# Kernel optimization log

Measured on AMD Instinct MI355X. Metric: run time of the kernel, lower is better.

The kernel has to match this reference:

```python
import jax, jax.numpy as jnp
import numpy as np

N_NODES = 50000
N_EDGES = 800000


def spmm(edge_src, edge_dst, edge_weight, h):
    # out[i] = sum over edges (src->dst=i) of w * h[src]  == adj @ h
    msgs = h[edge_src] * edge_weight[:, None]  # [E, D]
    return jax.ops.segment_sum(msgs, edge_dst, num_segments=N_NODES)


def setup_inputs() -> dict:
    key = jax.random.key(0)
    ks = jax.random.split(key, 12)
    x = jax.random.normal(ks[0], (N_NODES, 512), dtype=jnp.float32)
    edge_src = jax.random.randint(ks[1], (N_EDGES,), 0, N_NODES, dtype=jnp.int32)
    edge_dst = jax.random.randint(ks[2], (N_EDGES,), 0, N_NODES, dtype=jnp.int32)
    edge_weight = jax.random.uniform(ks[3], (N_EDGES,), dtype=jnp.float32)
    def init_w(k, fin, fout):
        s = 1.0 / np.sqrt(fout)
        return jax.random.uniform(k, (fin, fout), minval=-s, maxval=s, dtype=jnp.float32)
    W1 = init_w(ks[4], 512, 512); b1 = jnp.zeros((512,), jnp.float32)
    W2 = init_w(ks[5], 512, 256); b2 = jnp.zeros((256,), jnp.float32)
    W3 = init_w(ks[6], 256, 128); b3 = jnp.zeros((128,), jnp.float32)
    W4 = init_w(ks[7], 128, 64);  b4 = jnp.zeros((64,), jnp.float32)
    return {"x": x, "edge_src": edge_src, "edge_dst": edge_dst,
            "edge_weight": edge_weight, "W1": W1, "b1": b1, "W2": W2,
            "b2": b2, "W3": W3, "b3": b3, "W4": W4, "b4": b4}


def reference(x, edge_src, edge_dst, edge_weight, W1, b1, W2, b2, W3, b3, W4, b4):
    # GraphConvolution: out = adj @ (x @ W) + b ; dropout is identity in eval mode
    def gc(h, W, b):
        return spmm(edge_src, edge_dst, edge_weight, h @ W) + b
    h = jax.nn.relu(gc(x, W1, b1))
    h = jax.nn.relu(gc(h, W2, b2))
    h = jax.nn.relu(gc(h, W3, b3))
    emb = gc(h, W4, b4)
    return emb
```

## Files before the change

### kernel.cpp

```cpp
#include <hip/hip_runtime.h>

#define NN 50000
#define NE 800000
#define SCAN_BLOCKS 196

typedef __attribute__((ext_vector_type(8))) short short8;
typedef __attribute__((ext_vector_type(4))) float float4v;

struct us4 { unsigned short x, y, z, w; };
struct us8 { unsigned short v[8]; };

__device__ __forceinline__ unsigned short f2bf(float f) {
    unsigned u = __float_as_uint(f);
    unsigned r = (u + 0x7FFF + ((u >> 16) & 1)) >> 16;
    return (unsigned short)r;
}

__device__ __forceinline__ float bf2f(unsigned short u) {
    return __uint_as_float((unsigned)u << 16);
}

__device__ __forceinline__ void gload_lds16(const unsigned short* g, unsigned short* l) {
    __builtin_amdgcn_global_load_lds(
        (const __attribute__((address_space(1))) unsigned int*)g,
        (__attribute__((address_space(3))) unsigned int*)l,
        16, 0, 0);
}

template <int BM, int BN, int WM, int WN, int OUTBF>
__global__ __launch_bounds__(256) void gemm_mfma(const unsigned short* __restrict__ A,
                                                 const unsigned short* __restrict__ Bt,
                                                 void* __restrict__ Cv,
                                                 int N, int K, int M) {
    constexpr int BK = 32;
    constexpr int MT = WM / 16;
    constexpr int NT = WN / 16;
    constexpr int WCOLS = BN / WN;

    __shared__ __align__(16) unsigned short As[BM * BK];
    __shared__ __align__(16) unsigned short Bs[BN * BK];

    const int tid = threadIdx.x;
    const int lane = tid & 63;
    const int wid = tid >> 6;
    const int col16 = lane & 15;
    const int q = lane >> 4;
    const int wr = (wid / WCOLS) * WM;
    const int wc = (wid % WCOLS) * WN;
    const int rowBase = blockIdx.y * BM;
    const int colBase = blockIdx.x * BN;

    const int srow = lane >> 2;
    const int scol = (lane & 3) * 8;

    float4v acc[MT][NT];
#pragma unroll
    for (int t = 0; t < MT; ++t)
#pragma unroll
        for (int u = 0; u < NT; ++u)
            acc[t][u] = (float4v)0.f;

    for (int k0 = 0; k0 < K; k0 += BK) {
        __syncthreads();
#pragma unroll
        for (int l = wid; l < BM / 16; l += 4) {
            int row = rowBase + 16 * l + srow;
            row = row < N ? row : N - 1;
            gload_lds16(A + (size_t)row * K + k0 + scol, &As[l * 512]);
        }
#pragma unroll
        for (int l = wid; l < BN / 16; l += 4) {
            const int row = colBase + 16 * l + srow;
            gload_lds16(Bt + (size_t)row * K + k0 + scol, &Bs[l * 512]);
        }
        __syncthreads();

        short8 a[MT], b[NT];
#pragma unroll
        for (int t = 0; t < MT; ++t)
            a[t] = *(const short8*)&As[(wr + t * 16 + col16) * BK + q * 8];
#pragma unroll
        for (int u = 0; u < NT; ++u)
            b[u] = *(const short8*)&Bs[(wc + u * 16 + col16) * BK + q * 8];
#pragma unroll
        for (int t = 0; t < MT; ++t)
#pragma unroll
            for (int u = 0; u < NT; ++u)
                acc[t][u] = __builtin_amdgcn_mfma_f32_16x16x32_bf16(a[t], b[u], acc[t][u], 0, 0, 0);
    }

#pragma unroll
    for (int t = 0; t < MT; ++t) {
        const int row0 = rowBase + wr + t * 16 + q * 4;
#pragma unroll
        for (int u = 0; u < NT; ++u) {
            const int col = colBase + wc + u * 16 + col16;
#pragma unroll
            for (int r = 0; r < 4; ++r) {
                const int row = row0 + r;
                if (row < N) {
                    if (OUTBF)
                        ((unsigned short*)Cv)[(size_t)row * M + col] = f2bf(acc[t][u][r]);
                    else
                        ((float*)Cv)[(size_t)row * M + col] = acc[t][u][r];
                }
            }
        }
    }
}

__global__ void cvt_f32_bf16(const float* __restrict__ in, unsigned short* __restrict__ out,
                             long long n4) {
    long long i = (long long)blockIdx.x * blockDim.x + threadIdx.x;
    const long long stride = (long long)gridDim.x * blockDim.x;
    for (; i < n4; i += stride) {
        const float4 v = *(const float4*)&in[i * 4];
        us4 o = {f2bf(v.x), f2bf(v.y), f2bf(v.z), f2bf(v.w)};
        *(us4*)&out[i * 4] = o;
    }
}

__global__ void cvt_transpose(const float* __restrict__ W, unsigned short* __restrict__ Wt,
                              int K, int M) {
    int idx = blockIdx.x * blockDim.x + threadIdx.x;
    const int total = K * M;
    if (idx < total) {
        const int k = idx / M;
        const int m = idx % M;
        Wt[(size_t)m * K + k] = f2bf(W[idx]);
    }
}

__global__ void zero_counts(int* __restrict__ counts) {
    int i = blockIdx.x * blockDim.x + threadIdx.x;
    if (i < NN) counts[i] = 0;
}

__global__ void hist_dst(const int* __restrict__ dst, int* __restrict__ counts) {
    int i = blockIdx.x * blockDim.x + threadIdx.x;
    const int stride = gridDim.x * blockDim.x;
    for (; i < NE; i += stride) atomicAdd(&counts[dst[i]], 1);
}

__global__ __launch_bounds__(256) void scan_partial(const int* __restrict__ counts,
                                                    int* __restrict__ partials) {
    __shared__ int r[256];
    const int t = threadIdx.x;
    const int i = blockIdx.x * 256 + t;
    r[t] = (i < NN) ? counts[i] : 0;
    __syncthreads();
    for (int s = 128; s > 0; s >>= 1) {
        if (t < s) r[t] += r[t + s];
        __syncthreads();
    }
    if (t == 0) partials[blockIdx.x] = r[0];
}

__global__ __launch_bounds__(256) void scan_base(const int* __restrict__ partials,
                                                 int* __restrict__ bases,
                                                 int* __restrict__ offs) {
    __shared__ int s[256];
    const int t = threadIdx.x;
    const int v = (t < SCAN_BLOCKS) ? partials[t] : 0;
    s[t] = v;
    __syncthreads();
    for (int off = 1; off < 256; off <<= 1) {
        int x = (t >= off) ? s[t - off] : 0;
        __syncthreads();
        s[t] += x;
        __syncthreads();
    }
    if (t < SCAN_BLOCKS) bases[t] = s[t] - v;
    if (t == 255) offs[NN] = s[255];
}

__global__ __launch_bounds__(256) void scan_final(int* __restrict__ counts,
                                                  const int* __restrict__ bases,
                                                  int* __restrict__ offs) {
    __shared__ int s[256];
    const int t = threadIdx.x;
    const int i = blockIdx.x * 256 + t;
    const int v = (i < NN) ? counts[i] : 0;
    s[t] = v;
    __syncthreads();
    for (int off = 1; off < 256; off <<= 1) {
        int x = (t >= off) ? s[t - off] : 0;
        __syncthreads();
        s[t] += x;
        __syncthreads();
    }
    if (i < NN) {
        const int e = bases[blockIdx.x] + s[t] - v;
        offs[i] = e;
        counts[i] = e;
    }
}

__global__ void fill_csr(const int* __restrict__ src, const int* __restrict__ dst,
                         const float* __restrict__ w, int* __restrict__ cursor,
                         int* __restrict__ csr_src, float* __restrict__ csr_w) {
    int i = blockIdx.x * blockDim.x + threadIdx.x;
    const int stride = gridDim.x * blockDim.x;
    for (; i < NE; i += stride) {
        const int p = atomicAdd(&cursor[dst[i]], 1);
        csr_src[p] = src[i];
        csr_w[p] = w[i];
    }
}

template <int D, int RELU, int OUTBF>
__global__ __launch_bounds__(256) void spmm_gather(const int* __restrict__ offs,
                                                   const int* __restrict__ csr_src,
                                                   const float* __restrict__ csr_w,
                                                   const unsigned short* __restrict__ hp,
                                                   const float* __restrict__ bias,
                                                   void* __restrict__ outv) {
    constexpr int TPN = D / 8;
    constexpr int NPB = 256 / TPN;
    const int tid = threadIdx.x;
    const int node = blockIdx.x * NPB + tid / TPN;
    const int d = (tid % TPN) * 8;
    if (node >= NN) return;
    const int beg = offs[node];
    const int end = offs[node + 1];

    float acc[8] = {};
    int j = beg;
    for (; j + 2 <= end; j += 2) {
        const int s0 = csr_src[j];
        const int s1 = csr_src[j + 1];
        const float w0 = csr_w[j];
        const float w1 = csr_w[j + 1];
        const us8 h0 = *(const us8*)&hp[(long long)s0 * D + d];
        const us8 h1 = *(const us8*)&hp[(long long)s1 * D + d];
#pragma unroll
        for (int k = 0; k < 8; ++k)
            acc[k] += w0 * bf2f(h0.v[k]) + w1 * bf2f(h1.v[k]);
    }
    if (j < end) {
        const int s0 = csr_src[j];
        const float w0 = csr_w[j];
        const us8 h0 = *(const us8*)&hp[(long long)s0 * D + d];
#pragma unroll
        for (int k = 0; k < 8; ++k)
            acc[k] += w0 * bf2f(h0.v[k]);
    }
#pragma unroll
    for (int k = 0; k < 8; ++k) {
        acc[k] += bias[d + k];
        if (RELU) acc[k] = fmaxf(acc[k], 0.f);
    }
    if (OUTBF) {
        us8 o;
#pragma unroll
        for (int k = 0; k < 8; ++k) o.v[k] = f2bf(acc[k]);
        *(us8*)((unsigned short*)outv + (long long)node * D + d) = o;
    } else {
        float* op = (float*)outv + (long long)node * D + d;
        *(float4*)op = make_float4(acc[0], acc[1], acc[2], acc[3]);
        *(float4*)(op + 4) = make_float4(acc[4], acc[5], acc[6], acc[7]);
    }
}

extern "C" void kernel_launch(void* const* d_in, const int* in_sizes, int n_in,
                              void* d_out, int out_size, void* d_ws, size_t ws_size,
                              hipStream_t stream) {
    const float* x    = (const float*)d_in[0];
    const int*   esrc = (const int*)d_in[1];
    const int*   edst = (const int*)d_in[2];
    const float* ew   = (const float*)d_in[3];
    const float* W1 = (const float*)d_in[4];  const float* b1 = (const float*)d_in[5];
    const float* W2 = (const float*)d_in[6];  const float* b2 = (const float*)d_in[7];
    const float* W3 = (const float*)d_in[8];  const float* b3 = (const float*)d_in[9];
    const float* W4 = (const float*)d_in[10]; const float* b4 = (const float*)d_in[11];
    float* out = (float*)d_out;

    char* ws = (char*)d_ws;
    int*   offs    = (int*)ws;                    ws += (NN + 1) * sizeof(int);
    int*   counts  = (int*)ws;                    ws += NN * sizeof(int);
    int*   partials= (int*)ws;                    ws += 256 * sizeof(int);
    int*   bases   = (int*)ws;                    ws += 256 * sizeof(int);
    int*   csr_src = (int*)ws;                    ws += NE * sizeof(int);
    float* csr_w   = (float*)ws;                  ws += NE * sizeof(float);
    unsigned short* Wt1 = (unsigned short*)ws;    ws += 512 * 512 * sizeof(unsigned short);
    unsigned short* Wt2 = (unsigned short*)ws;    ws += 256 * 512 * sizeof(unsigned short);
    unsigned short* Wt3 = (unsigned short*)ws;    ws += 128 * 256 * sizeof(unsigned short);
    unsigned short* Wt4 = (unsigned short*)ws;    ws += 64 * 128 * sizeof(unsigned short);
    ws = (char*)(((uintptr_t)ws + 255) & ~(uintptr_t)255);
    unsigned short* tmp = (unsigned short*)ws;    ws += (size_t)NN * 512 * sizeof(unsigned short);
    ws = (char*)(((uintptr_t)ws + 255) & ~(uintptr_t)255);
    unsigned short* hb = (unsigned short*)ws;

    zero_counts<<<(NN + 255) / 256, 256, 0, stream>>>(counts);
    hist_dst<<<3125, 256, 0, stream>>>(edst, counts);
    scan_partial<<<SCAN_BLOCKS, 256, 0, stream>>>(counts, partials);
    scan_base<<<1, 256, 0, stream>>>(partials, bases, offs);
    scan_final<<<SCAN_BLOCKS, 256, 0, stream>>>(counts, bases, offs);
    fill_csr<<<3125, 256, 0, stream>>>(esrc, edst, ew, counts, csr_src, csr_w);

    cvt_f32_bf16<<<12800, 256, 0, stream>>>(x, hb, (long long)NN * 512 / 4);
    cvt_transpose<<<(512 * 512 + 255) / 256, 256, 0, stream>>>(W1, Wt1, 512, 512);
    cvt_transpose<<<(512 * 256 + 255) / 256, 256, 0, stream>>>(W2, Wt2, 512, 256);
    cvt_transpose<<<(256 * 128 + 255) / 256, 256, 0, stream>>>(W3, Wt3, 256, 128);
    cvt_transpose<<<(128 * 64 + 255) / 256, 256, 0, stream>>>(W4, Wt4, 128, 64);

    const int nby = (NN + 127) / 128;

    gemm_mfma<128, 128, 64, 64, 1><<<dim3(4, nby), 256, 0, stream>>>(hb, Wt1, tmp, NN, 512, 512);
    spmm_gather<512, 1, 1><<<NN / 4, 256, 0, stream>>>(offs, csr_src, csr_w, tmp, b1, hb);
    gemm_mfma<128, 128, 64, 64, 1><<<dim3(2, nby), 256, 0, stream>>>(hb, Wt2, tmp, NN, 512, 256);
    spmm_gather<256, 1, 1><<<NN / 8, 256, 0, stream>>>(offs, csr_src, csr_w, tmp, b2, hb);
    gemm_mfma<128, 128, 64, 64, 1><<<dim3(1, nby), 256, 0, stream>>>(hb, Wt3, tmp, NN, 256, 128);
    spmm_gather<128, 1, 1><<<NN / 16, 256, 0, stream>>>(offs, csr_src, csr_w, tmp, b3, hb);
    gemm_mfma<128, 64, 32, 64, 1><<<dim3(1, nby), 256, 0, stream>>>(hb, Wt4, tmp, NN, 128, 64);
    spmm_gather<64, 0, 0><<<(NN + 31) / 32, 256, 0, stream>>>(offs, csr_src, csr_w, tmp, b4, out);
}
```

Baseline: 622.5 us.

## Fuse input fp32-to-bf16 conversion into first GEMM, unroll gather, shrink small-layer tiles

The first GEMM now reads fp32 x directly and converts it to bf16 while staging into LDS, which removes the separate conversion kernel and its full write and re-read of a 50000x512 bf16 buffer. The SpMM gather loop is unrolled from 2 to 4 edges, giving more loads in flight per thread. The layer-3 and layer-4 GEMMs use 64-row tiles so more blocks launch. The fp32 A path uses ordinary global loads plus LDS stores instead of direct global-to-LDS loads, and the remainder loop may run up to three iterations.

```diff
diff --git a/kernel.cpp b/kernel.cpp
--- a/kernel.cpp
+++ b/kernel.cpp
@@ -27,8 +27,8 @@
         16, 0, 0);
 }
 
-template <int BM, int BN, int WM, int WN, int OUTBF>
-__global__ __launch_bounds__(256) void gemm_mfma(const unsigned short* __restrict__ A,
+template <int BM, int BN, int WM, int WN, int OUTBF, int AFP32>
+__global__ __launch_bounds__(256) void gemm_mfma(const void* __restrict__ Av,
                                                  const unsigned short* __restrict__ Bt,
                                                  void* __restrict__ Cv,
                                                  int N, int K, int M) {
@@ -66,7 +66,21 @@
         for (int l = wid; l < BM / 16; l += 4) {
             int row = rowBase + 16 * l + srow;
             row = row < N ? row : N - 1;
-            gload_lds16(A + (size_t)row * K + k0 + scol, &As[l * 512]);
+            if (AFP32) {
+                const float* Af = (const float*)Av;
+                const float4* p = (const float4*)(Af + (size_t)row * K + k0 + scol);
+                const float4 v0 = p[0];
+                const float4 v1 = p[1];
+                short8 o;
+                o[0] = (short)f2bf(v0.x); o[1] = (short)f2bf(v0.y);
+                o[2] = (short)f2bf(v0.z); o[3] = (short)f2bf(v0.w);
+                o[4] = (short)f2bf(v1.x); o[5] = (short)f2bf(v1.y);
+                o[6] = (short)f2bf(v1.z); o[7] = (short)f2bf(v1.w);
+                *(short8*)&As[l * 512 + lane * 8] = o;
+            } else {
+                const unsigned short* Ab = (const unsigned short*)Av;
+                gload_lds16(Ab + (size_t)row * K + k0 + scol, &As[l * 512]);
+            }
         }
 #pragma unroll
         for (int l = wid; l < BN / 16; l += 4) {
@@ -106,17 +120,6 @@
                 }
             }
         }
-    }
-}
-
-__global__ void cvt_f32_bf16(const float* __restrict__ in, unsigned short* __restrict__ out,
-                             long long n4) {
-    long long i = (long long)blockIdx.x * blockDim.x + threadIdx.x;
-    const long long stride = (long long)gridDim.x * blockDim.x;
-    for (; i < n4; i += stride) {
-        const float4 v = *(const float4*)&in[i * 4];
-        us4 o = {f2bf(v.x), f2bf(v.y), f2bf(v.z), f2bf(v.w)};
-        *(us4*)&out[i * 4] = o;
     }
 }
 
@@ -226,18 +229,25 @@
 
     float acc[8] = {};
     int j = beg;
-    for (; j + 2 <= end; j += 2) {
+    for (; j + 4 <= end; j += 4) {
         const int s0 = csr_src[j];
         const int s1 = csr_src[j + 1];
+        const int s2 = csr_src[j + 2];
+        const int s3 = csr_src[j + 3];
         const float w0 = csr_w[j];
         const float w1 = csr_w[j + 1];
+        const float w2 = csr_w[j + 2];
+        const float w3 = csr_w[j + 3];
         const us8 h0 = *(const us8*)&hp[(long long)s0 * D + d];
         const us8 h1 = *(const us8*)&hp[(long long)s1 * D + d];
+        const us8 h2 = *(const us8*)&hp[(long long)s2 * D + d];
+        const us8 h3 = *(const us8*)&hp[(long long)s3 * D + d];
 #pragma unroll
         for (int k = 0; k < 8; ++k)
-            acc[k] += w0 * bf2f(h0.v[k]) + w1 * bf2f(h1.v[k]);
-    }
-    if (j < end) {
+            acc[k] += w0 * bf2f(h0.v[k]) + w1 * bf2f(h1.v[k])
+                    + w2 * bf2f(h2.v[k]) + w3 * bf2f(h3.v[k]);
+    }
+    for (; j < end; ++j) {
         const int s0 = csr_src[j];
         const float w0 = csr_w[j];
         const us8 h0 = *(const us8*)&hp[(long long)s0 * D + d];
@@ -298,20 +308,20 @@
     scan_final<<<SCAN_BLOCKS, 256, 0, stream>>>(counts, bases, offs);
     fill_csr<<<3125, 256, 0, stream>>>(esrc, edst, ew, counts, csr_src, csr_w);
 
-    cvt_f32_bf16<<<12800, 256, 0, stream>>>(x, hb, (long long)NN * 512 / 4);
     cvt_transpose<<<(512 * 512 + 255) / 256, 256, 0, stream>>>(W1, Wt1, 512, 512);
     cvt_transpose<<<(512 * 256 + 255) / 256, 256, 0, stream>>>(W2, Wt2, 512, 256);
     cvt_transpose<<<(256 * 128 + 255) / 256, 256, 0, stream>>>(W3, Wt3, 256, 128);
     cvt_transpose<<<(128 * 64 + 255) / 256, 256, 0, stream>>>(W4, Wt4, 128, 64);
 
-    const int nby = (NN + 127) / 128;
-
-    gemm_mfma<128, 128, 64, 64, 1><<<dim3(4, nby), 256, 0, stream>>>(hb, Wt1, tmp, NN, 512, 512);
+    const int nby128 = (NN + 127) / 128;
+    const int nby64  = (NN + 63) / 64;
+
+    gemm_mfma<128, 128, 64, 64, 1, 1><<<dim3(4, nby128), 256, 0, stream>>>(x, Wt1, tmp, NN, 512, 512);
     spmm_gather<512, 1, 1><<<NN / 4, 256, 0, stream>>>(offs, csr_src, csr_w, tmp, b1, hb);
-    gemm_mfma<128, 128, 64, 64, 1><<<dim3(2, nby), 256, 0, stream>>>(hb, Wt2, tmp, NN, 512, 256);
+    gemm_mfma<128, 128, 64, 64, 1, 0><<<dim3(2, nby128), 256, 0, stream>>>(hb, Wt2, tmp, NN, 512, 256);
     spmm_gather<256, 1, 1><<<NN / 8, 256, 0, stream>>>(offs, csr_src, csr_w, tmp, b2, hb);
-    gemm_mfma<128, 128, 64, 64, 1><<<dim3(1, nby), 256, 0, stream>>>(hb, Wt3, tmp, NN, 256, 128);
+    gemm_mfma<64, 128, 32, 64, 1, 0><<<dim3(1, nby64), 256, 0, stream>>>(hb, Wt3, tmp, NN, 256, 128);
     spmm_gather<128, 1, 1><<<NN / 16, 256, 0, stream>>>(offs, csr_src, csr_w, tmp, b3, hb);
-    gemm_mfma<128, 64, 32, 64, 1><<<dim3(1, nby), 256, 0, stream>>>(hb, Wt4, tmp, NN, 128, 64);
+    gemm_mfma<64, 64, 32, 32, 1, 0><<<dim3(1, nby64), 256, 0, stream>>>(hb, Wt4, tmp, NN, 128, 64);
     spmm_gather<64, 0, 0><<<(NN + 31) / 32, 256, 0, stream>>>(offs, csr_src, csr_w, tmp, b4, out);
 }
```

Result: slower. 637.3 us (+2.4%).

## Split layer-1 SpMM into column halves, unroll gather by 4, retile small GEMMs

Applied to the files above, without the earlier changes.

The four weight convert-transpose launches become one kernel. The first-layer SpMM is split into two passes over 256-column halves so each pass has a smaller gather working set that may fit better in cache. The gather loop is unrolled to four edges so more loads are in flight. The last two GEMMs use smaller 64-row tiles to launch more blocks. The trade-off is that the CSR index and weight arrays are read twice for layer 1, and the smaller tiles get less data reuse.

```diff
diff --git a/kernel.cpp b/kernel.cpp
--- a/kernel.cpp
+++ b/kernel.cpp
@@ -120,15 +120,20 @@
     }
 }
 
-__global__ void cvt_transpose(const float* __restrict__ W, unsigned short* __restrict__ Wt,
-                              int K, int M) {
+__global__ void cvt_transpose_all(const float* __restrict__ W1, unsigned short* __restrict__ Wt1,
+                                  const float* __restrict__ W2, unsigned short* __restrict__ Wt2,
+                                  const float* __restrict__ W3, unsigned short* __restrict__ Wt3,
+                                  const float* __restrict__ W4, unsigned short* __restrict__ Wt4) {
     int idx = blockIdx.x * blockDim.x + threadIdx.x;
-    const int total = K * M;
-    if (idx < total) {
-        const int k = idx / M;
-        const int m = idx % M;
-        Wt[(size_t)m * K + k] = f2bf(W[idx]);
-    }
+    const float* W; unsigned short* Wt; int K, M;
+    if (idx < 262144)      { W = W1; Wt = Wt1; K = 512; M = 512; }
+    else if (idx < 393216) { idx -= 262144; W = W2; Wt = Wt2; K = 512; M = 256; }
+    else if (idx < 425984) { idx -= 393216; W = W3; Wt = Wt3; K = 256; M = 128; }
+    else if (idx < 434176) { idx -= 425984; W = W4; Wt = Wt4; K = 128; M = 64; }
+    else return;
+    const int k = idx / M;
+    const int m = idx % M;
+    Wt[(size_t)m * K + k] = f2bf(W[(size_t)k * M + m]);
 }
 
 __global__ void zero_counts(int* __restrict__ counts) {
@@ -214,33 +219,41 @@
                                                    const float* __restrict__ csr_w,
                                                    const unsigned short* __restrict__ hp,
                                                    const float* __restrict__ bias,
-                                                   void* __restrict__ outv) {
+                                                   void* __restrict__ outv,
+                                                   int dbase, int dstride) {
     constexpr int TPN = D / 8;
     constexpr int NPB = 256 / TPN;
     const int tid = threadIdx.x;
     const int node = blockIdx.x * NPB + tid / TPN;
-    const int d = (tid % TPN) * 8;
+    const int d = dbase + (tid % TPN) * 8;
     if (node >= NN) return;
     const int beg = offs[node];
     const int end = offs[node + 1];
 
     float acc[8] = {};
     int j = beg;
-    for (; j + 2 <= end; j += 2) {
+    for (; j + 4 <= end; j += 4) {
         const int s0 = csr_src[j];
         const int s1 = csr_src[j + 1];
+        const int s2 = csr_src[j + 2];
+        const int s3 = csr_src[j + 3];
         const float w0 = csr_w[j];
         const float w1 = csr_w[j + 1];
-        const us8 h0 = *(const us8*)&hp[(long long)s0 * D + d];
-        const us8 h1 = *(const us8*)&hp[(long long)s1 * D + d];
+        const float w2 = csr_w[j + 2];
+        const float w3 = csr_w[j + 3];
+        const us8 h0 = *(const us8*)&hp[(long long)s0 * dstride + d];
+        const us8 h1 = *(const us8*)&hp[(long long)s1 * dstride + d];
+        const us8 h2 = *(const us8*)&hp[(long long)s2 * dstride + d];
+        const us8 h3 = *(const us8*)&hp[(long long)s3 * dstride + d];
 #pragma unroll
         for (int k = 0; k < 8; ++k)
-            acc[k] += w0 * bf2f(h0.v[k]) + w1 * bf2f(h1.v[k]);
-    }
-    if (j < end) {
+            acc[k] += w0 * bf2f(h0.v[k]) + w1 * bf2f(h1.v[k])
+                    + w2 * bf2f(h2.v[k]) + w3 * bf2f(h3.v[k]);
+    }
+    for (; j < end; ++j) {
         const int s0 = csr_src[j];
         const float w0 = csr_w[j];
-        const us8 h0 = *(const us8*)&hp[(long long)s0 * D + d];
+        const us8 h0 = *(const us8*)&hp[(long long)s0 * dstride + d];
 #pragma unroll
         for (int k = 0; k < 8; ++k)
             acc[k] += w0 * bf2f(h0.v[k]);
@@ -254,9 +267,9 @@
         us8 o;
 #pragma unroll
         for (int k = 0; k < 8; ++k) o.v[k] = f2bf(acc[k]);
-        *(us8*)((unsigned short*)outv + (long long)node * D + d) = o;
+        *(us8*)((unsigned short*)outv + (long long)node * dstride + d) = o;
     } else {
-        float* op = (float*)outv + (long long)node * D + d;
+        float* op = (float*)outv + (long long)node * dstride + d;
         *(float4*)op = make_float4(acc[0], acc[1], acc[2], acc[3]);
         *(float4*)(op + 4) = make_float4(acc[4], acc[5], acc[6], acc[7]);
     }
@@ -299,19 +312,18 @@
     fill_csr<<<3125, 256, 0, stream>>>(esrc, edst, ew, counts, csr_src, csr_w);
 
     cvt_f32_bf16<<<12800, 256, 0, stream>>>(x, hb, (long long)NN * 512 / 4);
-    cvt_transpose<<<(512 * 512 + 255) / 256, 256, 0, stream>>>(W1, Wt1, 512, 512);
-    cvt_transpose<<<(512 * 256 + 255) / 256, 256, 0, stream>>>(W2, Wt2, 512, 256);
-    cvt_transpose<<<(256 * 128 + 255) / 256, 256, 0, stream>>>(W3, Wt3, 256, 128);
-    cvt_transpose<<<(128 * 64 + 255) / 256, 256, 0, stream>>>(W4, Wt4, 128, 64);
-
-    const int nby = (NN + 127) / 128;
-
-    gemm_mfma<128, 128, 64, 64, 1><<<dim3(4, nby), 256, 0, stream>>>(hb, Wt1, tmp, NN, 512, 512);
-    spmm_gather<512, 1, 1><<<NN / 4, 256, 0, stream>>>(offs, csr_src, csr_w, tmp, b1, hb);
-    gemm_mfma<128, 128, 64, 64, 1><<<dim3(2, nby), 256, 0, stream>>>(hb, Wt2, tmp, NN, 512, 256);
-    spmm_gather<256, 1, 1><<<NN / 8, 256, 0, stream>>>(offs, csr_src, csr_w, tmp, b2, hb);
-    gemm_mfma<128, 128, 64, 64, 1><<<dim3(1, nby), 256, 0, stream>>>(hb, Wt3, tmp, NN, 256, 128);
-    spmm_gather<128, 1, 1><<<NN / 16, 256, 0, stream>>>(offs, csr_src, csr_w, tmp, b3, hb);
-    gemm_mfma<128, 64, 32, 64, 1><<<dim3(1, nby), 256, 0, stream>>>(hb, Wt4, tmp, NN, 128, 64);
-    spmm_gather<64, 0, 0><<<(NN + 31) / 32, 256, 0, stream>>>(offs, csr_src, csr_w, tmp, b4, out);
-}
+    cvt_transpose_all<<<(434176 + 255) / 256, 256, 0, stream>>>(W1, Wt1, W2, Wt2, W3, Wt3, W4, Wt4);
+
+    const int nby128 = (NN + 127) / 128;
+    const int nby64  = (NN + 63) / 64;
+
+    gemm_mfma<128, 128, 64, 64, 1><<<dim3(4, nby128), 256, 0, stream>>>(hb, Wt1, tmp, NN, 512, 512);
+    spmm_gather<256, 1, 1><<<NN / 8, 256, 0, stream>>>(offs, csr_src, csr_w, tmp, b1, hb, 0, 512);
+    spmm_gather<256, 1, 1><<<NN / 8, 256, 0, stream>>>(offs, csr_src, csr_w, tmp, b1, hb, 256, 512);
+    gemm_mfma<128, 128, 64, 64, 1><<<dim3(2, nby128), 256, 0, stream>>>(hb, Wt2, tmp, NN, 512, 256);
+    spmm_gather<256, 1, 1><<<NN / 8, 256, 0, stream>>>(offs, csr_src, csr_w, tmp, b2, hb, 0, 256);
+    gemm_mfma<64, 128, 32, 64, 1><<<dim3(1, nby64), 256, 0, stream>>>(hb, Wt3, tmp, NN, 256, 128);
+    spmm_gather<128, 1, 1><<<NN / 16, 256, 0, stream>>>(offs, csr_src, csr_w, tmp, b3, hb, 0, 128);
+    gemm_mfma<64, 64, 32, 32, 1><<<dim3(1, nby64), 256, 0, stream>>>(hb, Wt4, tmp, NN, 128, 64);
+    spmm_gather<64, 0, 0><<<(NN + 31) / 32, 256, 0, stream>>>(offs, csr_src, csr_w, tmp, b4, out, 0, 64);
+}
```

Measured after the change: 609.6 us. 1.02x faster.
